# Performance work log

Hardware: AMD Instinct MI355X
Metric: run time of the kernel (lower is better)

## Reference

```python
import jax, jax.numpy as jnp
import numpy as np

N = 64        # n_nodes per graph
H = 128       # hidden channels (128x0e + 128x1o)
NB = 8        # radial bessel basis size
L = 2         # num_interactions
R_MAX = 5.0
AVG_NEIGH = 63.0
DIM = 3       # output vector dim
B = 64        # batch (vmapped)
T = 32        # time-embedding dim
S = 5         # num_species


def _edges(n):
    # fully-connected graph, no self loops (static shapes, jit-friendly)
    s, r = np.meshgrid(np.arange(n), np.arange(n), indexing='ij')
    m = s != r
    return jnp.asarray(s[m]), jnp.asarray(r[m])


def setup_inputs() -> dict:
    key = jax.random.key(0)
    ks = jax.random.split(key, 12)
    sc = 0.05
    return {
        'positions': jax.random.normal(ks[0], (B, N, 3), jnp.float32),
        'node_features': jax.random.randint(ks[1], (B, N), 0, S).astype(jnp.int64),
        'global_features': jax.random.normal(ks[2], (B, T), jnp.float32),
        'emb': jax.random.normal(ks[3], (S, H), jnp.float32) * sc,
        'Wt': jax.random.normal(ks[4], (T, H), jnp.float32) * sc,
        'Wr1': jax.random.normal(ks[5], (L, NB, H), jnp.float32) * sc,
        'Wr2': jax.random.normal(ks[6], (L, H, H), jnp.float32) * sc,
        'Wupd': jax.random.normal(ks[7], (L, H, H), jnp.float32) * sc,
        'Wmix': jax.random.normal(ks[8], (L, H, H), jnp.float32) * sc,
        'Wg1': jax.random.normal(ks[9], (H, H), jnp.float32) * sc,
        'Wg2': jax.random.normal(ks[10], (H, H), jnp.float32) * sc,
        'final_scaling': jnp.ones((), jnp.float32),
    }


def _call_single(pos, z, t, emb, Wt, Wr1, Wr2, Wupd, Wmix, Wg1, Wg2, final_scaling):
    snd, rcv = _edges(N)
    ev = pos[rcv] - pos[snd]                               # [E,3] edge vectors (gather)
    r = jnp.sqrt(jnp.sum(ev * ev, axis=-1) + 1e-12)        # [E]
    u = ev / r[:, None]                                    # unit directions
    # Bessel radial basis with cosine cutoff (r_max acts as soft radius graph)
    n = jnp.arange(1, NB + 1, dtype=pos.dtype)
    rb = jnp.sin(n * jnp.pi * r[:, None] / R_MAX) / r[:, None]   # [E,NB]
    fc = 0.5 * (jnp.cos(jnp.pi * r / R_MAX) + 1.0) * (r < R_MAX)
    rb = rb * fc[:, None]
    # node embedding from species + time embedding
    h = emb[z] + t @ Wt                                    # [N,H] scalar features
    v = jnp.zeros((N, H, DIM), pos.dtype)                  # vector (1o) features
    for l in range(L):
        w = jax.nn.silu(rb @ Wr1[l]) @ Wr2[l]              # [E,H] radial weights
        m0 = w * h[snd]                                    # [E,H] scalar messages
        m1 = m0[:, :, None] * u[:, None, :]                # [E,H,3] vector messages
        a0 = jax.ops.segment_sum(m0, rcv, num_segments=N) / AVG_NEIGH
        a1 = jax.ops.segment_sum(m1, rcv, num_segments=N) / AVG_NEIGH
        h = h + a0 @ Wupd[l]
        v = v + jnp.einsum('ngd,gh->nhd', a1, Wmix[l])
    # equivariant readout: scalar gate per channel contracts vector channels
    g = jax.nn.silu(h @ Wg1) @ Wg2                         # [N,H]
    out = jnp.einsum('nhd,nh->nd', v, g)                   # [N,3]
    return out * final_scaling


def reference(positions, node_features, global_features, emb, Wt, Wr1, Wr2, Wupd, Wmix, Wg1, Wg2, final_scaling):
    f = lambda p, z, t: _call_single(p, z, t, emb, Wt, Wr1, Wr2, Wupd, Wmix, Wg1, Wg2, final_scaling)
    return jax.vmap(f)(positions, node_features, global_features)
```

## Files before the change

kernel.cpp:

```cpp
#include <hip/hip_runtime.h>
#include <math.h>

#define NN 64
#define HH 128
#define NBB 8
#define TT 32
#define BB 64
#define NROW (BB * NN)
#define PLANE ((size_t)NROW * HH)
#define WR1OFF (8 * 16384)

typedef __attribute__((ext_vector_type(8))) short short8;
typedef __attribute__((ext_vector_type(4))) float f32x4;
typedef __attribute__((ext_vector_type(2))) unsigned int u32x2;

__device__ __forceinline__ float silu_f(float x) {
  return x * __builtin_amdgcn_rcpf(1.0f + __expf(-x));
}

__device__ __forceinline__ unsigned short bf1(float x) {
  __bf16 h = (__bf16)x;
  return *(unsigned short*)&h;
}
__device__ __forceinline__ unsigned bf2(float lo, float hi) {
  return (unsigned)bf1(lo) | ((unsigned)bf1(hi) << 16);
}

__device__ __forceinline__ void gemm8(
    const unsigned short (*sA)[136], const unsigned short* __restrict__ Bp,
    int w, int nlo, int quad, f32x4 C[2]) {
  const short8 z8 = {0, 0, 0, 0, 0, 0, 0, 0};
  short8 afr[4];
#pragma unroll
  for (int kt = 0; kt < 4; ++kt)
    afr[kt] = (nlo < 8) ? *(const short8*)&sA[nlo][kt * 32 + quad * 8] : z8;
#pragma unroll
  for (int nt = 0; nt < 2; ++nt)
#pragma unroll
    for (int kt = 0; kt < 4; ++kt) {
      short8 bfr = *(const short8*)&Bp[((kt * 128 + w * 32 + nt * 16 + nlo) * 4 + quad) * 8];
      C[nt] = __builtin_amdgcn_mfma_f32_16x16x32_bf16(afr[kt], bfr, C[nt], 0, 0, 0);
    }
}

__device__ __forceinline__ void gemm8_pre(
    const unsigned short (*sA)[136], const short8 Bf[4][2],
    int nlo, int quad, f32x4 C[2]) {
  const short8 z8 = {0, 0, 0, 0, 0, 0, 0, 0};
  short8 afr[4];
#pragma unroll
  for (int kt = 0; kt < 4; ++kt)
    afr[kt] = (nlo < 8) ? *(const short8*)&sA[nlo][kt * 32 + quad * 8] : z8;
#pragma unroll
  for (int nt = 0; nt < 2; ++nt)
#pragma unroll
    for (int kt = 0; kt < 4; ++kt)
      C[nt] = __builtin_amdgcn_mfma_f32_16x16x32_bf16(afr[kt], Bf[kt][nt], C[nt], 0, 0, 0);
}

__global__ __launch_bounds__(256) void k_init(
    const float* __restrict__ emb, const int* __restrict__ z,
    const float* __restrict__ gf, const float* __restrict__ Wt,
    const float* __restrict__ Wr1, const float* __restrict__ Wr2,
    const float* __restrict__ Wupd, const float* __restrict__ Wmix,
    const float* __restrict__ Wg1, const float* __restrict__ Wg2,
    float* __restrict__ h, unsigned short* __restrict__ Wpack) {
  __shared__ float tvec[HH];
  __shared__ int sz[NN];
  int b4 = blockIdx.x, tid = threadIdx.x;
  {
    int p2 = b4 * 256 + tid;
    int p = p2 * 2;
    int m = p >> 14;
    int j = p & 7;
    int q = (p >> 3) & 3;
    int n = (p >> 5) & 127;
    int kt = (p >> 12) & 3;
    int k = kt * 32 + q * 8 + j;
    const float* src;
    int base;
    if (m < 2) { src = Wr2; base = m * 16384; }
    else if (m < 4) { src = Wupd; base = (m - 2) * 16384; }
    else if (m < 6) { src = Wmix; base = (m - 4) * 16384; }
    else if (m == 6) { src = Wg1; base = 0; }
    else { src = Wg2; base = 0; }
    float v0 = src[base + k * 128 + n];
    float v1 = src[base + (k + 1) * 128 + n];
    *(unsigned*)&Wpack[p] = bf2(v0, v1);
  }
  if (tid < 32) {
    int e = b4 * 32 + tid;
    int l = e >> 12, p = e & 4095;
    int n = p >> 5, q = (p >> 3) & 3, j = p & 7;
    float val = (q == 0) ? Wr1[l * NBB * HH + j * HH + n] : 0.f;
    Wpack[WR1OFF + l * 4096 + p] = bf1(val);
  }
  if (b4 < 64) {
    int b = b4;
    if (tid < NN) sz[tid] = z[b * NN + tid];
    if (tid < HH) {
      float acc = 0.f;
#pragma unroll
      for (int k = 0; k < TT; ++k) acc += gf[b * TT + k] * Wt[k * HH + tid];
      tvec[tid] = acc;
    }
    __syncthreads();
    for (int i = tid; i < NN * HH; i += 256) {
      int n = i >> 7, c = i & 127;
      h[(size_t)b * NN * HH + i] = emb[sz[n] * HH + c] + tvec[c];
    }
  }
}

__global__ __launch_bounds__(256) void k_layer0(
    const float* __restrict__ pos, const float* __restrict__ hA,
    unsigned short* __restrict__ apout, const unsigned short* __restrict__ Wpack) {
  __shared__ __align__(16) unsigned short sh_S[NN][136];
  __shared__ __align__(16) unsigned short sh_M0T[4][32][72];
  __shared__ __align__(16) unsigned short sh_rbh[4][NN][8];
  __shared__ __align__(16) unsigned short sh_ub[4][4][NN];

  int blk = blockIdx.x;
  int b = blk >> 4, rp4 = blk & 15;
  int r0 = rp4 * 4;
  int tid = threadIdx.x;
  int w = tid >> 6, lane = tid & 63;
  int nlo = lane & 15, quad = lane >> 4;
  const short8 zero8 = {0, 0, 0, 0, 0, 0, 0, 0};

  f32x4 hbv[4][2];
#pragma unroll
  for (int mt = 0; mt < 4; ++mt)
#pragma unroll
    for (int nt = 0; nt < 2; ++nt)
#pragma unroll
      for (int reg = 0; reg < 4; ++reg)
        hbv[mt][nt][reg] =
            hA[((size_t)b * NN + mt * 16 + quad * 4 + reg) * HH + w * 32 + nt * 16 + nlo];

  const unsigned short* Wr1p = Wpack + WR1OFF;
  short8 bw[2];
#pragma unroll
  for (int nt = 0; nt < 2; ++nt)
    bw[nt] = *(const short8*)&Wr1p[((w * 32 + nt * 16 + nlo) * 4 + quad) * 8];
  const unsigned short* Bbase = Wpack;
  short8 bfr[4][2];
#pragma unroll
  for (int kt = 0; kt < 4; ++kt)
#pragma unroll
    for (int nt = 0; nt < 2; ++nt)
      bfr[kt][nt] = *(const short8*)&Bbase[((kt * 128 + w * 32 + nt * 16 + nlo) * 4 + quad) * 8];

  {
    int s = tid & 63;
    int ri4 = tid >> 6;
    int r = r0 + ri4;
    const float* pb = pos + b * NN * 3;
    float dx = pb[r * 3 + 0] - pb[s * 3 + 0];
    float dy = pb[r * 3 + 1] - pb[s * 3 + 1];
    float dz = pb[r * 3 + 2] - pb[s * 3 + 2];
    float rr = sqrtf(dx * dx + dy * dy + dz * dz + 1e-12f);
    float inv = __builtin_amdgcn_rcpf(rr);
    const float invAvg = 1.0f / 63.0f;
    float ia = inv * invAvg;
    sh_ub[ri4][0][s] = bf1(invAvg);
    sh_ub[ri4][1][s] = bf1(dx * ia);
    sh_ub[ri4][2][s] = bf1(dy * ia);
    sh_ub[ri4][3][s] = bf1(dz * ia);
    const float PI_OVER_5 = 0.628318530717958647692f;
    float fc = (s != r && rr < 5.0f) ? 0.5f * (__cosf(PI_OVER_5 * rr) + 1.0f) : 0.0f;
    float base = PI_OVER_5 * rr;
    float sc = inv * fc;
#pragma unroll
    for (int k0 = 0; k0 < 8; k0 += 4) {
      float v0 = __sinf((float)(k0 + 1) * base) * sc;
      float v1 = __sinf((float)(k0 + 2) * base) * sc;
      float v2 = __sinf((float)(k0 + 3) * base) * sc;
      float v3 = __sinf((float)(k0 + 4) * base) * sc;
      *(unsigned*)&sh_rbh[ri4][s][k0]     = bf2(v0, v1);
      *(unsigned*)&sh_rbh[ri4][s][k0 + 2] = bf2(v2, v3);
    }
  }
  __syncthreads();

#pragma unroll
  for (int rsel = 0; rsel < 4; ++rsel) {
#pragma unroll
    for (int mtp = 0; mtp < 2; ++mtp) {
      f32x4 Cs[2][2];
#pragma unroll
      for (int mi = 0; mi < 2; ++mi)
#pragma unroll
        for (int nt = 0; nt < 2; ++nt) Cs[mi][nt] = (f32x4){0.f, 0.f, 0.f, 0.f};
#pragma unroll
      for (int mi = 0; mi < 2; ++mi) {
        int mt = mtp * 2 + mi;
        short8 afr = (quad == 0) ? *(const short8*)&sh_rbh[rsel][mt * 16 + nlo][0] : zero8;
#pragma unroll
        for (int nt = 0; nt < 2; ++nt)
          Cs[mi][nt] = __builtin_amdgcn_mfma_f32_16x16x32_bf16(afr, bw[nt], Cs[mi][nt], 0, 0, 0);
      }
#pragma unroll
      for (int mi = 0; mi < 2; ++mi)
#pragma unroll
        for (int nt = 0; nt < 2; ++nt)
#pragma unroll
          for (int reg = 0; reg < 4; ++reg) {
            int s = (mtp * 2 + mi) * 16 + quad * 4 + reg;
            int c = w * 32 + nt * 16 + nlo;
            sh_S[s][c] = bf1(silu_f(Cs[mi][nt][reg]));
          }
    }
    __syncthreads();

#pragma unroll
    for (int mt = 0; mt < 4; ++mt) {
      short8 afr[4];
      int s_a = mt * 16 + nlo;
#pragma unroll
      for (int kt = 0; kt < 4; ++kt)
        afr[kt] = *(const short8*)&sh_S[s_a][kt * 32 + quad * 8];
#pragma unroll
      for (int nt = 0; nt < 2; ++nt) {
        f32x4 C = {0.f, 0.f, 0.f, 0.f};
#pragma unroll
        for (int kt = 0; kt < 4; ++kt)
          C = __builtin_amdgcn_mfma_f32_16x16x32_bf16(afr[kt], bfr[kt][nt], C, 0, 0, 0);
        f32x4 m0 = C * hbv[mt][nt];
        u32x2 pk;
        pk.x = bf2(m0[0], m0[1]);
        pk.y = bf2(m0[2], m0[3]);
        *(u32x2*)&sh_M0T[w][nt * 16 + nlo][mt * 16 + quad * 4] = pk;
      }
    }
    {
      short8 au[2];
#pragma unroll
      for (int kt = 0; kt < 2; ++kt)
        au[kt] = (nlo < 4) ? *(const short8*)&sh_ub[rsel][nlo][kt * 32 + quad * 8] : zero8;
      f32x4 Cu[2] = {{0, 0, 0, 0}, {0, 0, 0, 0}};
#pragma unroll
      for (int nt = 0; nt < 2; ++nt)
#pragma unroll
        for (int kt = 0; kt < 2; ++kt) {
          short8 bm = *(const short8*)&sh_M0T[w][nt * 16 + nlo][kt * 32 + quad * 8];
          Cu[nt] = __builtin_amdgcn_mfma_f32_16x16x32_bf16(au[kt], bm, Cu[nt], 0, 0, 0);
        }
      if (quad == 0) {
#pragma unroll
        for (int nt = 0; nt < 2; ++nt) {
          size_t base = (size_t)(b * NN + r0 + rsel) * HH + w * 32 + nt * 16 + nlo;
#pragma unroll
          for (int reg = 0; reg < 4; ++reg)
            apout[reg * PLANE + base] = bf1(Cu[nt][reg]);
        }
      }
    }
    if (rsel != 3) __syncthreads();
  }
}

__global__ __launch_bounds__(256) void k_fused(
    const float* __restrict__ pos, const float* __restrict__ hA,
    unsigned short* __restrict__ apbf, const unsigned short* __restrict__ Wpack,
    const float* __restrict__ fs, float* __restrict__ out) {
  __shared__ __align__(16) unsigned char smem[50688];
  unsigned short (*sh_S)[136]      = (unsigned short (*)[136])smem;
  unsigned short (*sh_M0T)[32][72] = (unsigned short (*)[32][72])(smem + 17408);
  unsigned short (*sh_rbh)[NN][8]  = (unsigned short (*)[NN][8])(smem + 35840);
  unsigned short (*sh_ub)[4][NN]   = (unsigned short (*)[4][NN])(smem + 39936);
  unsigned short (*sh_a47)[8][136] = (unsigned short (*)[8][136])(smem + 41984);

  int blk = blockIdx.x;
  int b = blk >> 3, u8 = blk & 7;
  int tid = threadIdx.x;
  int w = tid >> 6, lane = tid & 63;
  int nlo = lane & 15, quad = lane >> 4;
  const short8 zero8 = {0, 0, 0, 0, 0, 0, 0, 0};

  f32x4 hbv[4][2];
#pragma unroll
  for (int mt = 0; mt < 4; ++mt)
#pragma unroll
    for (int nt = 0; nt < 2; ++nt)
#pragma unroll
      for (int reg = 0; reg < 4; ++reg)
        hbv[mt][nt][reg] =
            hA[((size_t)b * NN + mt * 16 + quad * 4 + reg) * HH + w * 32 + nt * 16 + nlo];

  for (int i = tid; i < NN * 64; i += 256) {
    int s = i >> 6, c2 = (i & 63) * 2;
    *(unsigned*)&sh_S[s][c2] =
        *(const unsigned*)&apbf[((size_t)b * NN + s) * HH + c2];
  }
  __syncthreads();
  {
    const unsigned short* Bu = Wpack + 2 * 16384;
#pragma unroll
    for (int mt = 0; mt < 4; ++mt) {
      short8 afr[4];
#pragma unroll
      for (int kt = 0; kt < 4; ++kt)
        afr[kt] = *(const short8*)&sh_S[mt * 16 + nlo][kt * 32 + quad * 8];
#pragma unroll
      for (int nt = 0; nt < 2; ++nt)
#pragma unroll
        for (int kt = 0; kt < 4; ++kt) {
          short8 bfr2 = *(const short8*)&Bu[((kt * 128 + w * 32 + nt * 16 + nlo) * 4 + quad) * 8];
          hbv[mt][nt] = __builtin_amdgcn_mfma_f32_16x16x32_bf16(afr[kt], bfr2, hbv[mt][nt], 0, 0, 0);
        }
    }
  }
  __syncthreads();

  const unsigned short* Wr1p = Wpack + WR1OFF + 4096;
  short8 bw[2];
#pragma unroll
  for (int nt = 0; nt < 2; ++nt)
    bw[nt] = *(const short8*)&Wr1p[((w * 32 + nt * 16 + nlo) * 4 + quad) * 8];
  const unsigned short* Bbase = Wpack + 16384;
  short8 bfr[4][2];
#pragma unroll
  for (int kt = 0; kt < 4; ++kt)
#pragma unroll
    for (int nt = 0; nt < 2; ++nt)
      bfr[kt][nt] = *(const short8*)&Bbase[((kt * 128 + w * 32 + nt * 16 + nlo) * 4 + quad) * 8];

  for (int unit = 0; unit < 2; ++unit) {
    int r0 = u8 * 8 + unit * 4;

    {
      int s = tid & 63;
      int ri4 = tid >> 6;
      int r = r0 + ri4;
      const float* pb = pos + b * NN * 3;
      float dx = pb[r * 3 + 0] - pb[s * 3 + 0];
      float dy = pb[r * 3 + 1] - pb[s * 3 + 1];
      float dz = pb[r * 3 + 2] - pb[s * 3 + 2];
      float rr = sqrtf(dx * dx + dy * dy + dz * dz + 1e-12f);
      float inv = __builtin_amdgcn_rcpf(rr);
      const float invAvg = 1.0f / 63.0f;
      float ia = inv * invAvg;
      sh_ub[ri4][0][s] = bf1(invAvg);
      sh_ub[ri4][1][s] = bf1(dx * ia);
      sh_ub[ri4][2][s] = bf1(dy * ia);
      sh_ub[ri4][3][s] = bf1(dz * ia);
      const float PI_OVER_5 = 0.628318530717958647692f;
      float fc = (s != r && rr < 5.0f) ? 0.5f * (__cosf(PI_OVER_5 * rr) + 1.0f) : 0.0f;
      float base = PI_OVER_5 * rr;
      float sc = inv * fc;
#pragma unroll
      for (int k0 = 0; k0 < 8; k0 += 4) {
        float v0 = __sinf((float)(k0 + 1) * base) * sc;
        float v1 = __sinf((float)(k0 + 2) * base) * sc;
        float v2 = __sinf((float)(k0 + 3) * base) * sc;
        float v3 = __sinf((float)(k0 + 4) * base) * sc;
        *(unsigned*)&sh_rbh[ri4][s][k0]     = bf2(v0, v1);
        *(unsigned*)&sh_rbh[ri4][s][k0 + 2] = bf2(v2, v3);
      }
    }
    __syncthreads();

#pragma unroll
    for (int rsel = 0; rsel < 4; ++rsel) {
      int lr = unit * 4 + rsel;
#pragma unroll
      for (int mtp = 0; mtp < 2; ++mtp) {
        f32x4 Cs[2][2];
#pragma unroll
        for (int mi = 0; mi < 2; ++mi)
#pragma unroll
          for (int nt = 0; nt < 2; ++nt) Cs[mi][nt] = (f32x4){0.f, 0.f, 0.f, 0.f};
#pragma unroll
        for (int mi = 0; mi < 2; ++mi) {
          int mt = mtp * 2 + mi;
          short8 afr = (quad == 0) ? *(const short8*)&sh_rbh[rsel][mt * 16 + nlo][0] : zero8;
#pragma unroll
          for (int nt = 0; nt < 2; ++nt)
            Cs[mi][nt] = __builtin_amdgcn_mfma_f32_16x16x32_bf16(afr, bw[nt], Cs[mi][nt], 0, 0, 0);
        }
#pragma unroll
        for (int mi = 0; mi < 2; ++mi)
#pragma unroll
          for (int nt = 0; nt < 2; ++nt)
#pragma unroll
            for (int reg = 0; reg < 4; ++reg) {
              int s = (mtp * 2 + mi) * 16 + quad * 4 + reg;
              int c = w * 32 + nt * 16 + nlo;
              sh_S[s][c] = bf1(silu_f(Cs[mi][nt][reg]));
            }
      }
      __syncthreads();

#pragma unroll
      for (int mt = 0; mt < 4; ++mt) {
        short8 afr[4];
        int s_a = mt * 16 + nlo;
#pragma unroll
        for (int kt = 0; kt < 4; ++kt)
          afr[kt] = *(const short8*)&sh_S[s_a][kt * 32 + quad * 8];
#pragma unroll
        for (int nt = 0; nt < 2; ++nt) {
          f32x4 C = {0.f, 0.f, 0.f, 0.f};
#pragma unroll
          for (int kt = 0; kt < 4; ++kt)
            C = __builtin_amdgcn_mfma_f32_16x16x32_bf16(afr[kt], bfr[kt][nt], C, 0, 0, 0);
          f32x4 m0 = C * hbv[mt][nt];
          u32x2 pk;
          pk.x = bf2(m0[0], m0[1]);
          pk.y = bf2(m0[2], m0[3]);
          *(u32x2*)&sh_M0T[w][nt * 16 + nlo][mt * 16 + quad * 4] = pk;
        }
      }
      {
        short8 au[2];
#pragma unroll
        for (int kt = 0; kt < 2; ++kt)
          au[kt] = (nlo < 4) ? *(const short8*)&sh_ub[rsel][nlo][kt * 32 + quad * 8] : zero8;
        f32x4 Cu[2] = {{0, 0, 0, 0}, {0, 0, 0, 0}};
#pragma unroll
        for (int nt = 0; nt < 2; ++nt)
#pragma unroll
          for (int kt = 0; kt < 2; ++kt) {
            short8 bm = *(const short8*)&sh_M0T[w][nt * 16 + nlo][kt * 32 + quad * 8];
            Cu[nt] = __builtin_amdgcn_mfma_f32_16x16x32_bf16(au[kt], bm, Cu[nt], 0, 0, 0);
          }
        if (quad == 0) {
#pragma unroll
          for (int nt = 0; nt < 2; ++nt) {
            int c = w * 32 + nt * 16 + nlo;
#pragma unroll
            for (int reg = 0; reg < 4; ++reg)
              sh_a47[reg][lr][c] = bf1(Cu[nt][reg]);
          }
        }
      }
      __syncthreads();
    }
  }

  {
    unsigned short (*sh_a03)[8][136] = (unsigned short (*)[8][136])smem;
    unsigned short (*sh_h)[136]      = (unsigned short (*)[136])(smem + 8704);
    float (*red)[8][3]               = (float (*)[8][3])(smem + 8704 + 2176);
    int row0 = blk * 8;
    for (int i = tid; i < 4 * 8 * 64; i += 256) {
      int p = i >> 9, rr = (i >> 6) & 7, c2 = (i & 63) * 2;
      *(unsigned*)&sh_a03[p][rr][c2] =
          *(const unsigned*)&apbf[p * PLANE + (size_t)(row0 + rr) * HH + c2];
    }
    f32x4 Ch[2];
#pragma unroll
    for (int nt = 0; nt < 2; ++nt)
#pragma unroll
      for (int reg = 0; reg < 4; ++reg)
        Ch[nt][reg] = (quad < 2)
            ? hA[(size_t)(row0 + quad * 4 + reg) * HH + w * 32 + nt * 16 + nlo] : 0.f;
    __syncthreads();
    gemm8(sh_a03[0], Wpack + 2 * 16384, w, nlo, quad, Ch);
    gemm8(sh_a47[0], Wpack + 3 * 16384, w, nlo, quad, Ch);
    f32x4 Cx[2] = {{0,0,0,0},{0,0,0,0}};
    f32x4 Cy[2] = {{0,0,0,0},{0,0,0,0}};
    f32x4 Cz[2] = {{0,0,0,0},{0,0,0,0}};
    short8 Bmx[4][2];
#pragma unroll
    for (int kt = 0; kt < 4; ++kt)
#pragma unroll
      for (int nt = 0; nt < 2; ++nt)
        Bmx[kt][nt] = *(const short8*)&Wpack[4 * 16384 +
            ((kt * 128 + w * 32 + nt * 16 + nlo) * 4 + quad) * 8];
    gemm8_pre(sh_a03[1], Bmx, nlo, quad, Cx);
    gemm8_pre(sh_a03[2], Bmx, nlo, quad, Cy);
    gemm8_pre(sh_a03[3], Bmx, nlo, quad, Cz);
#pragma unroll
    for (int kt = 0; kt < 4; ++kt)
#pragma unroll
      for (int nt = 0; nt < 2; ++nt)
        Bmx[kt][nt] = *(const short8*)&Wpack[5 * 16384 +
            ((kt * 128 + w * 32 + nt * 16 + nlo) * 4 + quad) * 8];
    gemm8_pre(sh_a47[1], Bmx, nlo, quad, Cx);
    gemm8_pre(sh_a47[2], Bmx, nlo, quad, Cy);
    gemm8_pre(sh_a47[3], Bmx, nlo, quad, Cz);
    if (quad < 2) {
#pragma unroll
      for (int nt = 0; nt < 2; ++nt)
#pragma unroll
        for (int reg = 0; reg < 4; ++reg)
          sh_h[quad * 4 + reg][w * 32 + nt * 16 + nlo] = bf1(Ch[nt][reg]);
    }
    __syncthreads();
    unsigned short (*sh_q)[136] = sh_a03[0];
    f32x4 Cq[2] = {{0,0,0,0},{0,0,0,0}};
    gemm8(sh_h, Wpack + 6 * 16384, w, nlo, quad, Cq);
    if (quad < 2) {
#pragma unroll
      for (int nt = 0; nt < 2; ++nt)
#pragma unroll
        for (int reg = 0; reg < 4; ++reg)
          sh_q[quad * 4 + reg][w * 32 + nt * 16 + nlo] = bf1(silu_f(Cq[nt][reg]));
    }
    __syncthreads();
    f32x4 Cg[2] = {{0,0,0,0},{0,0,0,0}};
    gemm8(sh_q, Wpack + 7 * 16384, w, nlo, quad, Cg);
    float pr[3][4];
#pragma unroll
    for (int d = 0; d < 3; ++d)
#pragma unroll
      for (int reg = 0; reg < 4; ++reg) pr[d][reg] = 0.f;
#pragma unroll
    for (int nt = 0; nt < 2; ++nt)
#pragma unroll
      for (int reg = 0; reg < 4; ++reg) {
        float gv = Cg[nt][reg];
        pr[0][reg] += gv * Cx[nt][reg];
        pr[1][reg] += gv * Cy[nt][reg];
        pr[2][reg] += gv * Cz[nt][reg];
      }
#pragma unroll
    for (int off = 1; off < 16; off <<= 1)
#pragma unroll
      for (int d = 0; d < 3; ++d)
#pragma unroll
        for (int reg = 0; reg < 4; ++reg)
          pr[d][reg] += __shfl_xor(pr[d][reg], off);
    if (nlo == 0 && quad < 2) {
#pragma unroll
      for (int d = 0; d < 3; ++d)
#pragma unroll
        for (int reg = 0; reg < 4; ++reg)
          red[w][quad * 4 + reg][d] = pr[d][reg];
    }
    __syncthreads();
    if (tid < 24) {
      int row = tid / 3, d = tid % 3;
      float s = red[0][row][d] + red[1][row][d] + red[2][row][d] + red[3][row][d];
      out[(size_t)(row0 + row) * 3 + d] = s * fs[0];
    }
  }
}

extern "C" void kernel_launch(void* const* d_in, const int* in_sizes, int n_in,
                              void* d_out, int out_size, void* d_ws, size_t ws_size,
                              hipStream_t stream) {
  const float* pos  = (const float*)d_in[0];
  const int*   z    = (const int*)d_in[1];
  const float* gf   = (const float*)d_in[2];
  const float* emb  = (const float*)d_in[3];
  const float* Wt   = (const float*)d_in[4];
  const float* Wr1  = (const float*)d_in[5];
  const float* Wr2  = (const float*)d_in[6];
  const float* Wupd = (const float*)d_in[7];
  const float* Wmix = (const float*)d_in[8];
  const float* Wg1  = (const float*)d_in[9];
  const float* Wg2  = (const float*)d_in[10];
  const float* fs   = (const float*)d_in[11];
  float* out = (float*)d_out;

  float* ws = (float*)d_ws;
  float* hA = ws;
  unsigned short* apbf = (unsigned short*)(ws + PLANE);
  unsigned short* Wpack = (unsigned short*)(ws + 5 * PLANE);

  k_init<<<dim3(256), dim3(256), 0, stream>>>(emb, z, gf, Wt, Wr1, Wr2, Wupd,
                                              Wmix, Wg1, Wg2, hA, Wpack);
  k_layer0<<<dim3(BB * 16), dim3(256), 0, stream>>>(pos, hA, apbf, Wpack);
  k_fused<<<dim3(512), dim3(256), 0, stream>>>(pos, hA, apbf, Wpack, fs, out);
}
```

Baseline: 139.5 us.

## Double-buffer radial-weight stage and overlap with message GEMM in fused kernel

Splits the shared S buffer into two, so the silu(rb@Wr1) stage for the next receiver row runs before the Wr2 GEMM and vector contraction of the current row. This removes one barrier per row, and the edge-geometry stage for the next unit is folded into the last iteration. It also preloads the direction fragments for all four rows into registers and overlaps the first stageA with the initial h-update GEMM. In exchange, LDS use rises from about 50KB to 68KB per block and register pressure goes up, which may reduce occupancy.

```diff
diff --git a/kernel.cpp b/kernel.cpp
--- a/kernel.cpp
+++ b/kernel.cpp
@@ -264,12 +264,12 @@
     const float* __restrict__ pos, const float* __restrict__ hA,
     unsigned short* __restrict__ apbf, const unsigned short* __restrict__ Wpack,
     const float* __restrict__ fs, float* __restrict__ out) {
-  __shared__ __align__(16) unsigned char smem[50688];
-  unsigned short (*sh_S)[136]      = (unsigned short (*)[136])smem;
-  unsigned short (*sh_M0T)[32][72] = (unsigned short (*)[32][72])(smem + 17408);
-  unsigned short (*sh_rbh)[NN][8]  = (unsigned short (*)[NN][8])(smem + 35840);
-  unsigned short (*sh_ub)[4][NN]   = (unsigned short (*)[4][NN])(smem + 39936);
-  unsigned short (*sh_a47)[8][136] = (unsigned short (*)[8][136])(smem + 41984);
+  __shared__ __align__(16) unsigned char smem[68096];
+  unsigned short (*sh_S)[NN][136]  = (unsigned short (*)[NN][136])smem;
+  unsigned short (*sh_M0T)[32][72] = (unsigned short (*)[32][72])(smem + 34816);
+  unsigned short (*sh_rbh)[NN][8]  = (unsigned short (*)[NN][8])(smem + 53248);
+  unsigned short (*sh_ub)[4][NN]   = (unsigned short (*)[4][NN])(smem + 57344);
+  unsigned short (*sh_a47)[8][136] = (unsigned short (*)[8][136])(smem + 59392);
 
   int blk = blockIdx.x;
   int b = blk >> 3, u8 = blk & 7;
@@ -288,12 +288,45 @@
         hbv[mt][nt][reg] =
             hA[((size_t)b * NN + mt * 16 + quad * 4 + reg) * HH + w * 32 + nt * 16 + nlo];
 
+  auto stageA = [&](int unit) {
+    int s = tid & 63;
+    int ri4 = tid >> 6;
+    int r = u8 * 8 + unit * 4 + ri4;
+    const float* pb = pos + b * NN * 3;
+    float dx = pb[r * 3 + 0] - pb[s * 3 + 0];
+    float dy = pb[r * 3 + 1] - pb[s * 3 + 1];
+    float dz = pb[r * 3 + 2] - pb[s * 3 + 2];
+    float rr = sqrtf(dx * dx + dy * dy + dz * dz + 1e-12f);
+    float inv = __builtin_amdgcn_rcpf(rr);
+    const float invAvg = 1.0f / 63.0f;
+    float ia = inv * invAvg;
+    sh_ub[ri4][0][s] = bf1(invAvg);
+    sh_ub[ri4][1][s] = bf1(dx * ia);
+    sh_ub[ri4][2][s] = bf1(dy * ia);
+    sh_ub[ri4][3][s] = bf1(dz * ia);
+    const float PI_OVER_5 = 0.628318530717958647692f;
+    float fc = (s != r && rr < 5.0f) ? 0.5f * (__cosf(PI_OVER_5 * rr) + 1.0f) : 0.0f;
+    float base = PI_OVER_5 * rr;
+    float sc = inv * fc;
+#pragma unroll
+    for (int k0 = 0; k0 < 8; k0 += 4) {
+      float v0 = __sinf((float)(k0 + 1) * base) * sc;
+      float v1 = __sinf((float)(k0 + 2) * base) * sc;
+      float v2 = __sinf((float)(k0 + 3) * base) * sc;
+      float v3 = __sinf((float)(k0 + 4) * base) * sc;
+      *(unsigned*)&sh_rbh[ri4][s][k0]     = bf2(v0, v1);
+      *(unsigned*)&sh_rbh[ri4][s][k0 + 2] = bf2(v2, v3);
+    }
+  };
+
   for (int i = tid; i < NN * 64; i += 256) {
     int s = i >> 6, c2 = (i & 63) * 2;
-    *(unsigned*)&sh_S[s][c2] =
+    *(unsigned*)&sh_S[0][s][c2] =
         *(const unsigned*)&apbf[((size_t)b * NN + s) * HH + c2];
   }
+  stageA(0);
   __syncthreads();
+
   {
     const unsigned short* Bu = Wpack + 2 * 16384;
 #pragma unroll
@@ -301,7 +334,7 @@
       short8 afr[4];
 #pragma unroll
       for (int kt = 0; kt < 4; ++kt)
-        afr[kt] = *(const short8*)&sh_S[mt * 16 + nlo][kt * 32 + quad * 8];
+        afr[kt] = *(const short8*)&sh_S[0][mt * 16 + nlo][kt * 32 + quad * 8];
 #pragma unroll
       for (int nt = 0; nt < 2; ++nt)
 #pragma unroll
@@ -311,7 +344,6 @@
         }
     }
   }
-  __syncthreads();
 
   const unsigned short* Wr1p = Wpack + WR1OFF + 4096;
   short8 bw[2];
@@ -326,115 +358,92 @@
     for (int nt = 0; nt < 2; ++nt)
       bfr[kt][nt] = *(const short8*)&Bbase[((kt * 128 + w * 32 + nt * 16 + nlo) * 4 + quad) * 8];
 
+  auto stageB = [&](int rsel, int buf) {
+#pragma unroll
+    for (int mtp = 0; mtp < 2; ++mtp) {
+      f32x4 Cs[2][2];
+#pragma unroll
+      for (int mi = 0; mi < 2; ++mi)
+#pragma unroll
+        for (int nt = 0; nt < 2; ++nt) Cs[mi][nt] = (f32x4){0.f, 0.f, 0.f, 0.f};
+#pragma unroll
+      for (int mi = 0; mi < 2; ++mi) {
+        int mt = mtp * 2 + mi;
+        short8 afr = (quad == 0) ? *(const short8*)&sh_rbh[rsel][mt * 16 + nlo][0] : zero8;
+#pragma unroll
+        for (int nt = 0; nt < 2; ++nt)
+          Cs[mi][nt] = __builtin_amdgcn_mfma_f32_16x16x32_bf16(afr, bw[nt], Cs[mi][nt], 0, 0, 0);
+      }
+#pragma unroll
+      for (int mi = 0; mi < 2; ++mi)
+#pragma unroll
+        for (int nt = 0; nt < 2; ++nt)
+#pragma unroll
+          for (int reg = 0; reg < 4; ++reg) {
+            int s = (mtp * 2 + mi) * 16 + quad * 4 + reg;
+            int c = w * 32 + nt * 16 + nlo;
+            sh_S[buf][s][c] = bf1(silu_f(Cs[mi][nt][reg]));
+          }
+    }
+  };
+
+  auto mainG = [&](int buf, int lr, short8 au0, short8 au1) {
+#pragma unroll
+    for (int mt = 0; mt < 4; ++mt) {
+      short8 afr[4];
+      int s_a = mt * 16 + nlo;
+#pragma unroll
+      for (int kt = 0; kt < 4; ++kt)
+        afr[kt] = *(const short8*)&sh_S[buf][s_a][kt * 32 + quad * 8];
+#pragma unroll
+      for (int nt = 0; nt < 2; ++nt) {
+        f32x4 C = {0.f, 0.f, 0.f, 0.f};
+#pragma unroll
+        for (int kt = 0; kt < 4; ++kt)
+          C = __builtin_amdgcn_mfma_f32_16x16x32_bf16(afr[kt], bfr[kt][nt], C, 0, 0, 0);
+        f32x4 m0 = C * hbv[mt][nt];
+        u32x2 pk;
+        pk.x = bf2(m0[0], m0[1]);
+        pk.y = bf2(m0[2], m0[3]);
+        *(u32x2*)&sh_M0T[w][nt * 16 + nlo][mt * 16 + quad * 4] = pk;
+      }
+    }
+    f32x4 Cu[2] = {{0, 0, 0, 0}, {0, 0, 0, 0}};
+#pragma unroll
+    for (int nt = 0; nt < 2; ++nt) {
+      short8 bm0 = *(const short8*)&sh_M0T[w][nt * 16 + nlo][0 * 32 + quad * 8];
+      Cu[nt] = __builtin_amdgcn_mfma_f32_16x16x32_bf16(au0, bm0, Cu[nt], 0, 0, 0);
+      short8 bm1 = *(const short8*)&sh_M0T[w][nt * 16 + nlo][1 * 32 + quad * 8];
+      Cu[nt] = __builtin_amdgcn_mfma_f32_16x16x32_bf16(au1, bm1, Cu[nt], 0, 0, 0);
+    }
+    if (quad == 0) {
+#pragma unroll
+      for (int nt = 0; nt < 2; ++nt) {
+        int c = w * 32 + nt * 16 + nlo;
+#pragma unroll
+        for (int reg = 0; reg < 4; ++reg)
+          sh_a47[reg][lr][c] = bf1(Cu[nt][reg]);
+      }
+    }
+  };
+
   for (int unit = 0; unit < 2; ++unit) {
-    int r0 = u8 * 8 + unit * 4;
-
-    {
-      int s = tid & 63;
-      int ri4 = tid >> 6;
-      int r = r0 + ri4;
-      const float* pb = pos + b * NN * 3;
-      float dx = pb[r * 3 + 0] - pb[s * 3 + 0];
-      float dy = pb[r * 3 + 1] - pb[s * 3 + 1];
-      float dz = pb[r * 3 + 2] - pb[s * 3 + 2];
-      float rr = sqrtf(dx * dx + dy * dy + dz * dz + 1e-12f);
-      float inv = __builtin_amdgcn_rcpf(rr);
-      const float invAvg = 1.0f / 63.0f;
-      float ia = inv * invAvg;
-      sh_ub[ri4][0][s] = bf1(invAvg);
-      sh_ub[ri4][1][s] = bf1(dx * ia);
-      sh_ub[ri4][2][s] = bf1(dy * ia);
-      sh_ub[ri4][3][s] = bf1(dz * ia);
-      const float PI_OVER_5 = 0.628318530717958647692f;
-      float fc = (s != r && rr < 5.0f) ? 0.5f * (__cosf(PI_OVER_5 * rr) + 1.0f) : 0.0f;
-      float base = PI_OVER_5 * rr;
-      float sc = inv * fc;
-#pragma unroll
-      for (int k0 = 0; k0 < 8; k0 += 4) {
-        float v0 = __sinf((float)(k0 + 1) * base) * sc;
-        float v1 = __sinf((float)(k0 + 2) * base) * sc;
-        float v2 = __sinf((float)(k0 + 3) * base) * sc;
-        float v3 = __sinf((float)(k0 + 4) * base) * sc;
-        *(unsigned*)&sh_rbh[ri4][s][k0]     = bf2(v0, v1);
-        *(unsigned*)&sh_rbh[ri4][s][k0 + 2] = bf2(v2, v3);
-      }
-    }
-    __syncthreads();
-
-#pragma unroll
-    for (int rsel = 0; rsel < 4; ++rsel) {
-      int lr = unit * 4 + rsel;
-#pragma unroll
-      for (int mtp = 0; mtp < 2; ++mtp) {
-        f32x4 Cs[2][2];
-#pragma unroll
-        for (int mi = 0; mi < 2; ++mi)
-#pragma unroll
-          for (int nt = 0; nt < 2; ++nt) Cs[mi][nt] = (f32x4){0.f, 0.f, 0.f, 0.f};
-#pragma unroll
-        for (int mi = 0; mi < 2; ++mi) {
-          int mt = mtp * 2 + mi;
-          short8 afr = (quad == 0) ? *(const short8*)&sh_rbh[rsel][mt * 16 + nlo][0] : zero8;
-#pragma unroll
-          for (int nt = 0; nt < 2; ++nt)
-            Cs[mi][nt] = __builtin_amdgcn_mfma_f32_16x16x32_bf16(afr, bw[nt], Cs[mi][nt], 0, 0, 0);
-        }
-#pragma unroll
-        for (int mi = 0; mi < 2; ++mi)
-#pragma unroll
-          for (int nt = 0; nt < 2; ++nt)
-#pragma unroll
-            for (int reg = 0; reg < 4; ++reg) {
-              int s = (mtp * 2 + mi) * 16 + quad * 4 + reg;
-              int c = w * 32 + nt * 16 + nlo;
-              sh_S[s][c] = bf1(silu_f(Cs[mi][nt][reg]));
-            }
-      }
-      __syncthreads();
-
-#pragma unroll
-      for (int mt = 0; mt < 4; ++mt) {
-        short8 afr[4];
-        int s_a = mt * 16 + nlo;
-#pragma unroll
-        for (int kt = 0; kt < 4; ++kt)
-          afr[kt] = *(const short8*)&sh_S[s_a][kt * 32 + quad * 8];
-#pragma unroll
-        for (int nt = 0; nt < 2; ++nt) {
-          f32x4 C = {0.f, 0.f, 0.f, 0.f};
-#pragma unroll
-          for (int kt = 0; kt < 4; ++kt)
-            C = __builtin_amdgcn_mfma_f32_16x16x32_bf16(afr[kt], bfr[kt][nt], C, 0, 0, 0);
-          f32x4 m0 = C * hbv[mt][nt];
-          u32x2 pk;
-          pk.x = bf2(m0[0], m0[1]);
-          pk.y = bf2(m0[2], m0[3]);
-          *(u32x2*)&sh_M0T[w][nt * 16 + nlo][mt * 16 + quad * 4] = pk;
-        }
-      }
-      {
-        short8 au[2];
-#pragma unroll
-        for (int kt = 0; kt < 2; ++kt)
-          au[kt] = (nlo < 4) ? *(const short8*)&sh_ub[rsel][nlo][kt * 32 + quad * 8] : zero8;
-        f32x4 Cu[2] = {{0, 0, 0, 0}, {0, 0, 0, 0}};
-#pragma unroll
-        for (int nt = 0; nt < 2; ++nt)
-#pragma unroll
-          for (int kt = 0; kt < 2; ++kt) {
-            short8 bm = *(const short8*)&sh_M0T[w][nt * 16 + nlo][kt * 32 + quad * 8];
-            Cu[nt] = __builtin_amdgcn_mfma_f32_16x16x32_bf16(au[kt], bm, Cu[nt], 0, 0, 0);
-          }
-        if (quad == 0) {
-#pragma unroll
-          for (int nt = 0; nt < 2; ++nt) {
-            int c = w * 32 + nt * 16 + nlo;
-#pragma unroll
-            for (int reg = 0; reg < 4; ++reg)
-              sh_a47[reg][lr][c] = bf1(Cu[nt][reg]);
-          }
-        }
-      }
+    short8 auA[4][2];
+#pragma unroll
+    for (int rs = 0; rs < 4; ++rs)
+#pragma unroll
+      for (int kt = 0; kt < 2; ++kt)
+        auA[rs][kt] = (nlo < 4) ? *(const short8*)&sh_ub[rs][nlo][kt * 32 + quad * 8] : zero8;
+    __syncthreads();
+
+    stageB(0, 0);
+    __syncthreads();
+
+#pragma unroll
+    for (int k = 0; k < 4; ++k) {
+      if (k < 3) stageB(k + 1, (k + 1) & 1);
+      mainG(k & 1, unit * 4 + k, auA[k][0], auA[k][1]);
+      if (k == 3 && unit == 0) stageA(1);
       __syncthreads();
     }
   }
```

New measurement: 139.2 us. About the same (-0.2%).
